# Optimization experiments

Measured on AMD Instinct MI355X. Metric: run time of the kernel, lower is better.

The kernel has to match this reference:

```python
import jax, jax.numpy as jnp
import numpy as np

N_ATOMS = 100000
M_NBRS = 12
ATOM_F = 64
NBR_F = 41
BN_EPS = 1e-5


def setup_inputs() -> dict:
    key = jax.random.key(0)
    k1, k2, k3, k4, k5 = jax.random.split(key, 5)
    atom_fea = jax.random.normal(k1, (N_ATOMS, ATOM_F), dtype=jnp.float32)
    nbr_fea = jax.random.normal(k2, (N_ATOMS, M_NBRS, NBR_F), dtype=jnp.float32)
    # fc_full: Linear(2*atom + nbr -> 2*atom), torch layout [out, in]
    in_dim = 2 * ATOM_F + NBR_F
    out_dim = 2 * ATOM_F
    W = jax.random.normal(k3, (out_dim, in_dim), dtype=jnp.float32) * (1.0 / np.sqrt(in_dim))
    b = jax.random.normal(k4, (out_dim,), dtype=jnp.float32) * 0.01
    gamma = jnp.ones((ATOM_F,), dtype=jnp.float32)
    beta = jnp.zeros((ATOM_F,), dtype=jnp.float32)
    nbr_idx = jax.random.randint(k5, (N_ATOMS, M_NBRS), 0, N_ATOMS, dtype=jnp.int32)
    return {"atom_fea": atom_fea, "nbr_fea": nbr_fea, "W": W, "b": b,
            "gamma": gamma, "beta": beta, "nbr_idx": nbr_idx}


def reference(atom_fea, nbr_fea, W, b, gamma, beta, nbr_idx):
    N, M = nbr_idx.shape
    F = atom_fea.shape[1]
    # gather neighbor atom features: [N, M, F]
    nbr_atom_fea = atom_fea[nbr_idx]
    # broadcast self features: [N, M, F]
    self_fea = jnp.broadcast_to(atom_fea[:, None, :], (N, M, F))
    # concat [self, nbr_atom, edge] -> [N, M, 2F + nbr_F]
    total_fea = jnp.concatenate([self_fea, nbr_atom_fea, nbr_fea], axis=2)
    # shared linear: [N, M, 2F]
    total_fea = jnp.einsum('nmi,oi->nmo', total_fea, W) + b
    filter_fea, core_fea = jnp.split(total_fea, 2, axis=2)
    # gated message, sum over neighbors -> [N, F]
    nbr_msg = (jax.nn.sigmoid(filter_fea) * jax.nn.softplus(core_fea)).sum(axis=1)
    # BatchNorm1d (training mode: batch stats, biased variance)
    x = atom_fea + nbr_msg
    mean = x.mean(axis=0)
    var = x.var(axis=0)
    x_hat = (x - mean) * jax.lax.rsqrt(var + BN_EPS)
    out = x_hat * gamma + beta
    return jax.nn.softplus(out)
```

## Files before the change

### kernel.cpp

```cpp
#include <hip/hip_runtime.h>

#define N_ATOMS 100000
#define M_NBRS 12
#define ATOM_F 64
#define NBR_F 41
#define OUT_DIM 128
#define IN_DIM 169
#define N_GROUPS (N_ATOMS / 16)

typedef __attribute__((ext_vector_type(8))) short short8;
typedef __attribute__((ext_vector_type(4))) float f32x4;
typedef __attribute__((ext_vector_type(2))) unsigned u32x2;
typedef __attribute__((ext_vector_type(4))) unsigned u32x4;

__device__ __forceinline__ unsigned short f2bf(float f) {
    union { float f; unsigned u; } v; v.f = f;
    unsigned u = v.u;
    return (unsigned short)((u + 0x7fffu + ((u >> 16) & 1u)) >> 16);
}
__device__ __forceinline__ unsigned cvt_pk(float a, float b) {
    unsigned r;
    asm("v_cvt_pk_bf16_f32 %0, %1, %2" : "=v"(r) : "v"(a), "v"(b));
    return r;
}
__device__ __forceinline__ float softplus_f(float x) {
    return fmaxf(x, 0.f) + __logf(1.f + __expf(-fabsf(x)));
}
__device__ __forceinline__ float sigmoid_f(float x) {
    return __fdividef(1.f, 1.f + __expf(-x));
}

#define WS_STRIDE 72
__global__ __launch_bounds__(256, 4) void k_prep(
    const float* __restrict__ atom, const float* __restrict__ W,
    const float* __restrict__ bias, unsigned* __restrict__ abf_u32,
    unsigned* __restrict__ A1P, float* __restrict__ SUM)
{
    __shared__ unsigned short Ws[128 * WS_STRIDE];
    __shared__ unsigned Ap[4 * 16 * 36];
    __shared__ unsigned T2[4][16 * 68];
    const int tid = threadIdx.x;
    const int w = tid >> 6, l = tid & 63;
    const int r = l & 15, g = l >> 4;

    if (blockIdx.x == 0 && tid < 128) SUM[tid] = 0.f;

    for (int e = tid; e < 128 * 64; e += 256) {
        int col = e >> 6, k = e & 63;
        Ws[col * WS_STRIDE + k] = f2bf(W[col * IN_DIM + k]);
    }
    __syncthreads();

    short8 bf[8][2];
    #pragma unroll
    for (int nt = 0; nt < 8; ++nt)
      #pragma unroll
      for (int kk = 0; kk < 2; ++kk) {
            int col = nt * 16 + r;
            union { u32x4 u; short8 s; } u;
            u.u = *reinterpret_cast<const u32x4*>(&Ws[col * WS_STRIDE + kk * 32 + g * 8]);
            bf[nt][kk] = u.s;
      }
    float bb[8];
    #pragma unroll
    for (int nt = 0; nt < 8; ++nt) bb[nt] = bias[nt * 16 + r];

    const int totalw = gridDim.x * 4;
    const int gw = blockIdx.x * 4 + w;
    const int step = totalw * 16;
    const int T = (N_ATOMS + step - 1) / step;
    unsigned* Aw = &Ap[w * 16 * 36];
    unsigned* Tw = T2[w];

    for (int t = 0; t < T; ++t) {
        int base = gw * 16 + t * step;
        #pragma unroll
        for (int sub = 0; sub < 4; ++sub) {
            int chunk = g * 4 + sub;
            int a = base + r;
            float4 v = make_float4(0.f, 0.f, 0.f, 0.f);
            if (a < N_ATOMS)
                v = reinterpret_cast<const float4*>(atom)[a * 16 + chunk];
            Aw[r * 36 + chunk * 2]     = cvt_pk(v.x, v.y);
            Aw[r * 36 + chunk * 2 + 1] = cvt_pk(v.z, v.w);
        }
        {
            int al = l >> 2, part = l & 3;
            int a = base + al;
            if (a < N_ATOMS) {
                u32x4 d0 = *reinterpret_cast<const u32x4*>(&Aw[al * 36 + part * 8]);
                u32x4 d1 = *reinterpret_cast<const u32x4*>(&Aw[al * 36 + part * 8 + 4]);
                *reinterpret_cast<u32x4*>(&abf_u32[(size_t)a * 32 + part * 8]) = d0;
                *reinterpret_cast<u32x4*>(&abf_u32[(size_t)a * 32 + part * 8 + 4]) = d1;
            }
        }
        short8 af[2];
        #pragma unroll
        for (int kk = 0; kk < 2; ++kk) {
            union { u32x4 u; short8 s; } u;
            u.u = *reinterpret_cast<const u32x4*>(&Aw[r * 36 + kk * 16 + g * 4]);
            af[kk] = u.s;
        }
        #pragma unroll
        for (int nt = 0; nt < 4; ++nt) {
            f32x4 accf = {0.f,0.f,0.f,0.f}, accc = {0.f,0.f,0.f,0.f};
            accf = __builtin_amdgcn_mfma_f32_16x16x32_bf16(af[0], bf[nt][0],   accf, 0,0,0);
            accf = __builtin_amdgcn_mfma_f32_16x16x32_bf16(af[1], bf[nt][1],   accf, 0,0,0);
            accc = __builtin_amdgcn_mfma_f32_16x16x32_bf16(af[0], bf[nt+4][0], accc, 0,0,0);
            accc = __builtin_amdgcn_mfma_f32_16x16x32_bf16(af[1], bf[nt+4][1], accc, 0,0,0);
            #pragma unroll
            for (int r4 = 0; r4 < 4; ++r4) {
                int row = g * 4 + r4;
                Tw[row * 68 + r * 4 + nt] = cvt_pk(accf[r4] + bb[nt], accc[r4] + bb[nt + 4]);
            }
        }
        {
            int al = l >> 2, part = l & 3;
            int a = base + al;
            if (a < N_ATOMS) {
                #pragma unroll
                for (int q = 0; q < 4; ++q) {
                    u32x4 d = *reinterpret_cast<const u32x4*>(&Tw[al * 68 + part * 16 + q * 4]);
                    *reinterpret_cast<u32x4*>(&A1P[(size_t)a * 64 + part * 16 + q * 4]) = d;
                }
            }
        }
    }
}

#define BS_STRIDE 136

struct TBuf { u32x2 ga[4]; float f0[4], f1[4], f2[4], f3[4]; };

__device__ __forceinline__ TBuf load_data(
    const unsigned* __restrict__ abf, const float* __restrict__ nbr,
    int base, int m, const int* jj, int c, int g)
{
    TBuf b;
    #pragma unroll
    for (int rr = 0; rr < 4; ++rr) {
        b.ga[rr] = *reinterpret_cast<const u32x2*>(abf + (size_t)jj[rr] * 32 + 2 * c);
        const float* ep = nbr + ((size_t)(base + rr * 4 + g) * M_NBRS + m) * NBR_F + 4 * c;
        bool c10 = (c < 10);
        b.f0[rr] = (c < 11) ? ep[0] : 0.f;
        b.f1[rr] = c10 ? ep[1] : 0.f;
        b.f2[rr] = c10 ? ep[2] : 0.f;
        b.f3[rr] = c10 ? ep[3] : 0.f;
    }
    return b;
}

__global__ __launch_bounds__(256, 3) void k_msg(
    const float* __restrict__ atom, const float* __restrict__ nbr,
    const float* __restrict__ W, const int* __restrict__ idx,
    const unsigned* __restrict__ abf, const unsigned* __restrict__ A1P,
    float* __restrict__ X, float* __restrict__ SUM)
{
    __shared__ __align__(16) unsigned short Bs[128 * BS_STRIDE];
    __shared__ __align__(16) unsigned Au[4 * 16 * 68];
    const int tid = threadIdx.x;
    const int w = tid >> 6, l = tid & 63;
    const int c = l & 15, g = l >> 4;
    unsigned* Aw = &Au[w * 16 * 68];

    for (int e = tid; e < 128 * BS_STRIDE / 2; e += 256)
        reinterpret_cast<unsigned*>(Bs)[e] = 0u;
    __syncthreads();
    for (int e = tid; e < 128 * 105; e += 256) {
        unsigned col = (unsigned)e / 105u;
        unsigned k = (unsigned)e - col * 105u;
        Bs[col * BS_STRIDE + k] = f2bf(W[col * IN_DIM + 64 + k]);
    }
    __syncthreads();

    const int gw = blockIdx.x * 4 + w;
    float sum_p[4] = {0.f,0.f,0.f,0.f}, sq_p[4] = {0.f,0.f,0.f,0.f};

    if (gw < N_GROUPS) {
        const int base = gw * 16;
        u32x4 a1q[4];
        #pragma unroll
        for (int r4 = 0; r4 < 4; ++r4)
            a1q[r4] = *reinterpret_cast<const u32x4*>(
                &A1P[(size_t)(base + g * 4 + r4) * 64 + c * 4]);

        float gs[4][4];
        #pragma unroll
        for (int r4 = 0; r4 < 4; ++r4)
          #pragma unroll
          for (int p = 0; p < 4; ++p) gs[r4][p] = 0.f;

        unsigned bofs = (unsigned)(c * BS_STRIDE + g * 8) * 2u;

        int jn[4];
        TBuf buf;
        {
            int j0[4];
            #pragma unroll
            for (int rr = 0; rr < 4; ++rr)
                j0[rr] = idx[(base + rr * 4 + g) * M_NBRS + 0];
            buf = load_data(abf, nbr, base, 0, j0, c, g);
        }
        #pragma unroll
        for (int rr = 0; rr < 4; ++rr)
            jn[rr] = idx[(base + rr * 4 + g) * M_NBRS + 1];

        #pragma unroll 1
        for (int m = 0; m < M_NBRS; ++m) {
            asm volatile("" : "+v"(bofs));
            #pragma unroll
            for (int rr = 0; rr < 4; ++rr) {
                int r = rr * 4 + g;
                *reinterpret_cast<u32x2*>(Aw + r * 68 + 2 * c) = buf.ga[rr];
                u32x2 e;
                e[0] = cvt_pk(buf.f0[rr], buf.f1[rr]);
                e[1] = cvt_pk(buf.f2[rr], buf.f3[rr]);
                *reinterpret_cast<u32x2*>(Aw + r * 68 + 32 + 2 * c) = e;
            }
            if (m + 1 < M_NBRS) {
                buf = load_data(abf, nbr, base, m + 1, jn, c, g);
                if (m + 2 < M_NBRS) {
                    #pragma unroll
                    for (int rr = 0; rr < 4; ++rr)
                        jn[rr] = idx[(base + rr * 4 + g) * M_NBRS + m + 2];
                }
            }
            short8 af[4];
            #pragma unroll
            for (int kk = 0; kk < 4; ++kk) {
                union { u32x4 u; short8 s; } u;
                u.u = *reinterpret_cast<const u32x4*>(&Aw[c * 68 + kk * 16 + g * 4]);
                af[kk] = u.s;
            }
            const char* bsb = reinterpret_cast<const char*>(Bs);
            #pragma unroll
            for (int p = 0; p < 4; ++p) {
                f32x4 accf, accc;
                #pragma unroll
                for (int r4 = 0; r4 < 4; ++r4) {
                    unsigned a1 = a1q[r4][p];
                    accf[r4] = __uint_as_float(a1 << 16);
                    accc[r4] = __uint_as_float(a1 & 0xffff0000u);
                }
                #pragma unroll
                for (int kk = 0; kk < 4; ++kk) {
                    union { u32x4 u; short8 s; } uf, uc;
                    uf.u = *reinterpret_cast<const u32x4*>(
                        bsb + bofs + (p * 16 * BS_STRIDE + kk * 32) * 2);
                    uc.u = *reinterpret_cast<const u32x4*>(
                        bsb + bofs + ((p + 4) * 16 * BS_STRIDE + kk * 32) * 2);
                    accf = __builtin_amdgcn_mfma_f32_16x16x32_bf16(af[kk], uf.s, accf, 0,0,0);
                    accc = __builtin_amdgcn_mfma_f32_16x16x32_bf16(af[kk], uc.s, accc, 0,0,0);
                }
                #pragma unroll
                for (int r4 = 0; r4 < 4; ++r4)
                    gs[r4][p] += sigmoid_f(accf[r4]) * softplus_f(accc[r4]);
            }
        }
        #pragma unroll
        for (int r4 = 0; r4 < 4; ++r4) {
            int o = (base + g * 4 + r4) * ATOM_F + c;
            #pragma unroll
            for (int p = 0; p < 4; ++p) {
                float x = atom[o + p * 16] + gs[r4][p];
                X[o + p * 16] = x;
                sum_p[p] += x;
                sq_p[p] += x * x;
            }
        }
    }

    #pragma unroll
    for (int p = 0; p < 4; ++p) {
        sum_p[p] += __shfl_xor(sum_p[p], 16, 64);
        sum_p[p] += __shfl_xor(sum_p[p], 32, 64);
        sq_p[p]  += __shfl_xor(sq_p[p], 16, 64);
        sq_p[p]  += __shfl_xor(sq_p[p], 32, 64);
    }
    __syncthreads();
    float* Rs = reinterpret_cast<float*>(Bs);
    if (g == 0) {
        #pragma unroll
        for (int p = 0; p < 4; ++p) {
            Rs[w * 128 + p * 16 + c] = sum_p[p];
            Rs[512 + w * 128 + p * 16 + c] = sq_p[p];
        }
    }
    __syncthreads();
    if (tid < 128) {
        int q = tid & 63;
        int o = (tid >> 6) * 512;
        float v = Rs[o + q] + Rs[o + 128 + q] + Rs[o + 256 + q] + Rs[o + 384 + q];
        atomicAdd(&SUM[tid], v);
    }
}

__global__ void k_stats2(const float* __restrict__ SUM, const float* __restrict__ gamma,
                         const float* __restrict__ beta, float* __restrict__ MS)
{
    int t = threadIdx.x;
    float mean = SUM[t] * (1.f / N_ATOMS);
    float msq  = SUM[64 + t] * (1.f / N_ATOMS);
    float var  = msq - mean * mean;
    float inv  = rsqrtf(var + 1e-5f);
    float sc   = inv * gamma[t];
    float sh   = beta[t] - mean * sc;
    MS[t] = sc;
    MS[64 + t] = sh;
}

__global__ void k_final(float* __restrict__ X, const float* __restrict__ MS)
{
    int q = blockIdx.x * 256 + threadIdx.x;
    const float4* MS4 = reinterpret_cast<const float4*>(MS);
    float4 x = reinterpret_cast<const float4*>(X)[q];
    float4 sc = MS4[q & 15];
    float4 sh = MS4[16 + (q & 15)];
    float4 o;
    o.x = softplus_f(x.x * sc.x + sh.x);
    o.y = softplus_f(x.y * sc.y + sh.y);
    o.z = softplus_f(x.z * sc.z + sh.z);
    o.w = softplus_f(x.w * sc.w + sh.w);
    reinterpret_cast<float4*>(X)[q] = o;
}

extern "C" void kernel_launch(void* const* d_in, const int* in_sizes, int n_in,
                              void* d_out, int out_size, void* d_ws, size_t ws_size,
                              hipStream_t stream)
{
    const float* atom  = (const float*)d_in[0];
    const float* nbr   = (const float*)d_in[1];
    const float* W     = (const float*)d_in[2];
    const float* bias  = (const float*)d_in[3];
    const float* gamma = (const float*)d_in[4];
    const float* beta  = (const float*)d_in[5];
    const int*   idx   = (const int*)d_in[6];
    float* X = (float*)d_out;

    char* ws = (char*)d_ws;
    unsigned* abf = (unsigned*)ws;
    unsigned* A1P = (unsigned*)(ws + (size_t)N_ATOMS * 32 * 4);
    float* SUM    = (float*)(ws + (size_t)N_ATOMS * 32 * 4
                                + (size_t)N_ATOMS * 64 * 4);
    float* MS     = SUM + 128;

    const int msg_blocks = (N_GROUPS + 3) / 4;
    hipLaunchKernelGGL(k_prep,   dim3(512),        dim3(256), 0, stream, atom, W, bias, abf, A1P, SUM);
    hipLaunchKernelGGL(k_msg,    dim3(msg_blocks), dim3(256), 0, stream, atom, nbr, W, idx, abf, A1P, X, SUM);
    hipLaunchKernelGGL(k_stats2, dim3(1),          dim3(64),  0, stream, SUM, gamma, beta, MS);
    hipLaunchKernelGGL(k_final,  dim3(6250),       dim3(256), 0, stream, X, MS);
}
```

Before: 414.5 us.

## Load MFMA A-fragments directly from global and pre-swizzle weight fragments in LDS

The message kernel now loads each neighbor's bf16 atom features and edge features directly into MFMA A-operand registers, with one atom row per lane column. This removes the per-neighbor LDS staging writes and reads. Weights are stored in LDS already laid out as per-lane fragments, which drops the padded stride and the zero-fill pass, lowers LDS use and allows occupancy 4. The prep kernel writes A1P in fragment order and launches one wave per 16-atom group instead of a grid-stride loop. The risks are more uncoalesced scattered global loads per lane, with edge loads of 8 floats each, and higher register pressure.

```diff
diff --git a/kernel.cpp b/kernel.cpp
--- a/kernel.cpp
+++ b/kernel.cpp
@@ -10,14 +10,8 @@
 
 typedef __attribute__((ext_vector_type(8))) short short8;
 typedef __attribute__((ext_vector_type(4))) float f32x4;
-typedef __attribute__((ext_vector_type(2))) unsigned u32x2;
 typedef __attribute__((ext_vector_type(4))) unsigned u32x4;
 
-__device__ __forceinline__ unsigned short f2bf(float f) {
-    union { float f; unsigned u; } v; v.f = f;
-    unsigned u = v.u;
-    return (unsigned short)((u + 0x7fffu + ((u >> 16) & 1u)) >> 16);
-}
 __device__ __forceinline__ unsigned cvt_pk(float a, float b) {
     unsigned r;
     asm("v_cvt_pk_bf16_f32 %0, %1, %2" : "=v"(r) : "v"(a), "v"(b));
@@ -30,146 +24,122 @@
     return __fdividef(1.f, 1.f + __expf(-x));
 }
 
-#define WS_STRIDE 72
 __global__ __launch_bounds__(256, 4) void k_prep(
     const float* __restrict__ atom, const float* __restrict__ W,
     const float* __restrict__ bias, unsigned* __restrict__ abf_u32,
     unsigned* __restrict__ A1P, float* __restrict__ SUM)
 {
-    __shared__ unsigned short Ws[128 * WS_STRIDE];
-    __shared__ unsigned Ap[4 * 16 * 36];
-    __shared__ unsigned T2[4][16 * 68];
+    __shared__ __align__(16) unsigned BFp[16 * 64 * 4];
     const int tid = threadIdx.x;
     const int w = tid >> 6, l = tid & 63;
     const int r = l & 15, g = l >> 4;
 
     if (blockIdx.x == 0 && tid < 128) SUM[tid] = 0.f;
 
-    for (int e = tid; e < 128 * 64; e += 256) {
-        int col = e >> 6, k = e & 63;
-        Ws[col * WS_STRIDE + k] = f2bf(W[col * IN_DIM + k]);
+    #pragma unroll
+    for (int s = 0; s < 4; ++s) {
+        int f = s * 4 + w;
+        int nt = f >> 1, kk = f & 1;
+        int col = nt * 16 + r;
+        int kbase = kk * 32 + g * 8;
+        const float* wp = W + col * IN_DIM + kbase;
+        u32x4 pk;
+        pk[0] = cvt_pk(wp[0], wp[1]); pk[1] = cvt_pk(wp[2], wp[3]);
+        pk[2] = cvt_pk(wp[4], wp[5]); pk[3] = cvt_pk(wp[6], wp[7]);
+        *reinterpret_cast<u32x4*>(&BFp[(f * 64 + l) * 4]) = pk;
     }
     __syncthreads();
 
-    short8 bf[8][2];
-    #pragma unroll
-    for (int nt = 0; nt < 8; ++nt)
-      #pragma unroll
-      for (int kk = 0; kk < 2; ++kk) {
-            int col = nt * 16 + r;
-            union { u32x4 u; short8 s; } u;
-            u.u = *reinterpret_cast<const u32x4*>(&Ws[col * WS_STRIDE + kk * 32 + g * 8]);
-            bf[nt][kk] = u.s;
-      }
+    const int gw = blockIdx.x * 4 + w;
+    if (gw >= N_GROUPS) return;
+    const int base = gw * 16;
+
     float bb[8];
     #pragma unroll
     for (int nt = 0; nt < 8; ++nt) bb[nt] = bias[nt * 16 + r];
 
-    const int totalw = gridDim.x * 4;
-    const int gw = blockIdx.x * 4 + w;
-    const int step = totalw * 16;
-    const int T = (N_ATOMS + step - 1) / step;
-    unsigned* Aw = &Ap[w * 16 * 36];
-    unsigned* Tw = T2[w];
-
-    for (int t = 0; t < T; ++t) {
-        int base = gw * 16 + t * step;
-        #pragma unroll
-        for (int sub = 0; sub < 4; ++sub) {
-            int chunk = g * 4 + sub;
-            int a = base + r;
-            float4 v = make_float4(0.f, 0.f, 0.f, 0.f);
-            if (a < N_ATOMS)
-                v = reinterpret_cast<const float4*>(atom)[a * 16 + chunk];
-            Aw[r * 36 + chunk * 2]     = cvt_pk(v.x, v.y);
-            Aw[r * 36 + chunk * 2 + 1] = cvt_pk(v.z, v.w);
-        }
-        {
-            int al = l >> 2, part = l & 3;
-            int a = base + al;
-            if (a < N_ATOMS) {
-                u32x4 d0 = *reinterpret_cast<const u32x4*>(&Aw[al * 36 + part * 8]);
-                u32x4 d1 = *reinterpret_cast<const u32x4*>(&Aw[al * 36 + part * 8 + 4]);
-                *reinterpret_cast<u32x4*>(&abf_u32[(size_t)a * 32 + part * 8]) = d0;
-                *reinterpret_cast<u32x4*>(&abf_u32[(size_t)a * 32 + part * 8 + 4]) = d1;
-            }
-        }
-        short8 af[2];
+    union { u32x4 u; short8 s; } af[2];
+    #pragma unroll
+    for (int kk = 0; kk < 2; ++kk) {
+        const float4* ap = reinterpret_cast<const float4*>(atom)
+                           + (size_t)(base + r) * 16 + kk * 8 + g * 2;
+        float4 v0 = ap[0], v1 = ap[1];
+        af[kk].u[0] = cvt_pk(v0.x, v0.y); af[kk].u[1] = cvt_pk(v0.z, v0.w);
+        af[kk].u[2] = cvt_pk(v1.x, v1.y); af[kk].u[3] = cvt_pk(v1.z, v1.w);
+        *reinterpret_cast<u32x4*>(&abf_u32[(size_t)(base + r) * 32 + kk * 16 + g * 4])
+            = af[kk].u;
+    }
+
+    u32x4 outp[4];
+    #pragma unroll
+    for (int nt = 0; nt < 4; ++nt) {
+        f32x4 accf = {0.f,0.f,0.f,0.f}, accc = {0.f,0.f,0.f,0.f};
         #pragma unroll
         for (int kk = 0; kk < 2; ++kk) {
-            union { u32x4 u; short8 s; } u;
-            u.u = *reinterpret_cast<const u32x4*>(&Aw[r * 36 + kk * 16 + g * 4]);
-            af[kk] = u.s;
-        }
-        #pragma unroll
-        for (int nt = 0; nt < 4; ++nt) {
-            f32x4 accf = {0.f,0.f,0.f,0.f}, accc = {0.f,0.f,0.f,0.f};
-            accf = __builtin_amdgcn_mfma_f32_16x16x32_bf16(af[0], bf[nt][0],   accf, 0,0,0);
-            accf = __builtin_amdgcn_mfma_f32_16x16x32_bf16(af[1], bf[nt][1],   accf, 0,0,0);
-            accc = __builtin_amdgcn_mfma_f32_16x16x32_bf16(af[0], bf[nt+4][0], accc, 0,0,0);
-            accc = __builtin_amdgcn_mfma_f32_16x16x32_bf16(af[1], bf[nt+4][1], accc, 0,0,0);
-            #pragma unroll
-            for (int r4 = 0; r4 < 4; ++r4) {
-                int row = g * 4 + r4;
-                Tw[row * 68 + r * 4 + nt] = cvt_pk(accf[r4] + bb[nt], accc[r4] + bb[nt + 4]);
-            }
-        }
-        {
-            int al = l >> 2, part = l & 3;
-            int a = base + al;
-            if (a < N_ATOMS) {
-                #pragma unroll
-                for (int q = 0; q < 4; ++q) {
-                    u32x4 d = *reinterpret_cast<const u32x4*>(&Tw[al * 68 + part * 16 + q * 4]);
-                    *reinterpret_cast<u32x4*>(&A1P[(size_t)a * 64 + part * 16 + q * 4]) = d;
-                }
-            }
-        }
-    }
-}
-
-#define BS_STRIDE 136
-
-struct TBuf { u32x2 ga[4]; float f0[4], f1[4], f2[4], f3[4]; };
-
-__device__ __forceinline__ TBuf load_data(
-    const unsigned* __restrict__ abf, const float* __restrict__ nbr,
-    int base, int m, const int* jj, int c, int g)
-{
-    TBuf b;
-    #pragma unroll
-    for (int rr = 0; rr < 4; ++rr) {
-        b.ga[rr] = *reinterpret_cast<const u32x2*>(abf + (size_t)jj[rr] * 32 + 2 * c);
-        const float* ep = nbr + ((size_t)(base + rr * 4 + g) * M_NBRS + m) * NBR_F + 4 * c;
-        bool c10 = (c < 10);
-        b.f0[rr] = (c < 11) ? ep[0] : 0.f;
-        b.f1[rr] = c10 ? ep[1] : 0.f;
-        b.f2[rr] = c10 ? ep[2] : 0.f;
-        b.f3[rr] = c10 ? ep[3] : 0.f;
+            union { u32x4 u; short8 s; } uf, uc;
+            uf.u = *reinterpret_cast<const u32x4*>(&BFp[((nt * 2 + kk) * 64 + l) * 4]);
+            uc.u = *reinterpret_cast<const u32x4*>(&BFp[(((nt + 4) * 2 + kk) * 64 + l) * 4]);
+            accf = __builtin_amdgcn_mfma_f32_16x16x32_bf16(af[kk].s, uf.s, accf, 0,0,0);
+            accc = __builtin_amdgcn_mfma_f32_16x16x32_bf16(af[kk].s, uc.s, accc, 0,0,0);
+        }
+        #pragma unroll
+        for (int r4 = 0; r4 < 4; ++r4)
+            outp[r4][nt] = cvt_pk(accf[r4] + bb[nt], accc[r4] + bb[nt + 4]);
+    }
+    #pragma unroll
+    for (int r4 = 0; r4 < 4; ++r4)
+        *reinterpret_cast<u32x4*>(&A1P[(size_t)gw * 1024 + r4 * 256 + l * 4]) = outp[r4];
+}
+
+struct EBuf { unsigned p2[4]; unsigned p3[4]; };
+
+__device__ __forceinline__ EBuf load_edges(const float* __restrict__ ep, int g)
+{
+    EBuf b;
+    float v[8];
+    #pragma unroll
+    for (int j = 0; j < 8; ++j) v[j] = ep[g * 8 + j];
+    b.p2[0] = cvt_pk(v[0], v[1]); b.p2[1] = cvt_pk(v[2], v[3]);
+    b.p2[2] = cvt_pk(v[4], v[5]); b.p2[3] = cvt_pk(v[6], v[7]);
+    b.p3[0] = b.p3[1] = b.p3[2] = b.p3[3] = 0u;
+    if (g == 0) {
+        float u[8];
+        #pragma unroll
+        for (int j = 0; j < 8; ++j) u[j] = ep[32 + j];
+        b.p3[0] = cvt_pk(u[0], u[1]); b.p3[1] = cvt_pk(u[2], u[3]);
+        b.p3[2] = cvt_pk(u[4], u[5]); b.p3[3] = cvt_pk(u[6], u[7]);
+    } else if (g == 1) {
+        b.p3[0] = cvt_pk(ep[40], 0.f);
     }
     return b;
 }
 
-__global__ __launch_bounds__(256, 3) void k_msg(
+__global__ __launch_bounds__(256, 4) void k_msg(
     const float* __restrict__ atom, const float* __restrict__ nbr,
     const float* __restrict__ W, const int* __restrict__ idx,
     const unsigned* __restrict__ abf, const unsigned* __restrict__ A1P,
     float* __restrict__ X, float* __restrict__ SUM)
 {
-    __shared__ __align__(16) unsigned short Bs[128 * BS_STRIDE];
-    __shared__ __align__(16) unsigned Au[4 * 16 * 68];
+    __shared__ __align__(16) unsigned BF[32 * 64 * 4];
     const int tid = threadIdx.x;
     const int w = tid >> 6, l = tid & 63;
     const int c = l & 15, g = l >> 4;
-    unsigned* Aw = &Au[w * 16 * 68];
-
-    for (int e = tid; e < 128 * BS_STRIDE / 2; e += 256)
-        reinterpret_cast<unsigned*>(Bs)[e] = 0u;
-    __syncthreads();
-    for (int e = tid; e < 128 * 105; e += 256) {
-        unsigned col = (unsigned)e / 105u;
-        unsigned k = (unsigned)e - col * 105u;
-        Bs[col * BS_STRIDE + k] = f2bf(W[col * IN_DIM + 64 + k]);
+
+    #pragma unroll
+    for (int s = 0; s < 8; ++s) {
+        int f = s * 4 + w;
+        int nt = f >> 2, kk = f & 3;
+        int col = nt * 16 + c;
+        int kbase = kk * 32 + g * 8;
+        const float* wp = W + col * IN_DIM + 64 + kbase;
+        u32x4 pk;
+        float v[8];
+        #pragma unroll
+        for (int j = 0; j < 8; ++j)
+            v[j] = (kbase + j < 105) ? wp[j] : 0.f;
+        pk[0] = cvt_pk(v[0], v[1]); pk[1] = cvt_pk(v[2], v[3]);
+        pk[2] = cvt_pk(v[4], v[5]); pk[3] = cvt_pk(v[6], v[7]);
+        *reinterpret_cast<u32x4*>(&BF[(f * 64 + l) * 4]) = pk;
     }
     __syncthreads();
 
@@ -182,7 +152,7 @@
         #pragma unroll
         for (int r4 = 0; r4 < 4; ++r4)
             a1q[r4] = *reinterpret_cast<const u32x4*>(
-                &A1P[(size_t)(base + g * 4 + r4) * 64 + c * 4]);
+                &A1P[(size_t)gw * 1024 + r4 * 256 + l * 4]);
 
         float gs[4][4];
         #pragma unroll
@@ -190,72 +160,62 @@
           #pragma unroll
           for (int p = 0; p < 4; ++p) gs[r4][p] = 0.f;
 
-        unsigned bofs = (unsigned)(c * BS_STRIDE + g * 8) * 2u;
-
-        int jn[4];
-        TBuf buf;
+        const int irow = (base + c) * M_NBRS;
+        const float* erow = nbr + (size_t)irow * NBR_F;
+
+        unsigned bofs = (unsigned)l * 16u;
+
+        u32x4 at0, at1, at0n, at1n;
+        EBuf eb, ebn;
+        int jn;
         {
-            int j0[4];
-            #pragma unroll
-            for (int rr = 0; rr < 4; ++rr)
-                j0[rr] = idx[(base + rr * 4 + g) * M_NBRS + 0];
-            buf = load_data(abf, nbr, base, 0, j0, c, g);
-        }
-        #pragma unroll
-        for (int rr = 0; rr < 4; ++rr)
-            jn[rr] = idx[(base + rr * 4 + g) * M_NBRS + 1];
+            int j0 = idx[irow];
+            at0 = *reinterpret_cast<const u32x4*>(abf + (size_t)j0 * 32 + g * 4);
+            at1 = *reinterpret_cast<const u32x4*>(abf + (size_t)j0 * 32 + 16 + g * 4);
+            eb = load_edges(erow, g);
+        }
+        jn = idx[irow + 1];
 
         #pragma unroll 1
         for (int m = 0; m < M_NBRS; ++m) {
+            if (m + 1 < M_NBRS) {
+                at0n = *reinterpret_cast<const u32x4*>(abf + (size_t)jn * 32 + g * 4);
+                at1n = *reinterpret_cast<const u32x4*>(abf + (size_t)jn * 32 + 16 + g * 4);
+                ebn = load_edges(erow + (m + 1) * NBR_F, g);
+                if (m + 2 < M_NBRS) jn = idx[irow + m + 2];
+            }
             asm volatile("" : "+v"(bofs));
-            #pragma unroll
-            for (int rr = 0; rr < 4; ++rr) {
-                int r = rr * 4 + g;
-                *reinterpret_cast<u32x2*>(Aw + r * 68 + 2 * c) = buf.ga[rr];
-                u32x2 e;
-                e[0] = cvt_pk(buf.f0[rr], buf.f1[rr]);
-                e[1] = cvt_pk(buf.f2[rr], buf.f3[rr]);
-                *reinterpret_cast<u32x2*>(Aw + r * 68 + 32 + 2 * c) = e;
-            }
-            if (m + 1 < M_NBRS) {
-                buf = load_data(abf, nbr, base, m + 1, jn, c, g);
-                if (m + 2 < M_NBRS) {
-                    #pragma unroll
-                    for (int rr = 0; rr < 4; ++rr)
-                        jn[rr] = idx[(base + rr * 4 + g) * M_NBRS + m + 2];
-                }
-            }
-            short8 af[4];
-            #pragma unroll
-            for (int kk = 0; kk < 4; ++kk) {
-                union { u32x4 u; short8 s; } u;
-                u.u = *reinterpret_cast<const u32x4*>(&Aw[c * 68 + kk * 16 + g * 4]);
-                af[kk] = u.s;
-            }
-            const char* bsb = reinterpret_cast<const char*>(Bs);
+            const char* bsb = reinterpret_cast<const char*>(BF);
+            union { u32x4 u; short8 s; } a0, a1, a2, a3;
+            a0.u = at0; a1.u = at1;
+            a2.u[0] = eb.p2[0]; a2.u[1] = eb.p2[1]; a2.u[2] = eb.p2[2]; a2.u[3] = eb.p2[3];
+            a3.u[0] = eb.p3[0]; a3.u[1] = eb.p3[1]; a3.u[2] = eb.p3[2]; a3.u[3] = eb.p3[3];
             #pragma unroll
             for (int p = 0; p < 4; ++p) {
                 f32x4 accf, accc;
                 #pragma unroll
                 for (int r4 = 0; r4 < 4; ++r4) {
-                    unsigned a1 = a1q[r4][p];
-                    accf[r4] = __uint_as_float(a1 << 16);
-                    accc[r4] = __uint_as_float(a1 & 0xffff0000u);
+                    unsigned v = a1q[r4][p];
+                    accf[r4] = __uint_as_float(v << 16);
+                    accc[r4] = __uint_as_float(v & 0xffff0000u);
                 }
                 #pragma unroll
                 for (int kk = 0; kk < 4; ++kk) {
                     union { u32x4 u; short8 s; } uf, uc;
                     uf.u = *reinterpret_cast<const u32x4*>(
-                        bsb + bofs + (p * 16 * BS_STRIDE + kk * 32) * 2);
+                        bsb + bofs + (unsigned)((p * 4 + kk) * 64 * 16));
                     uc.u = *reinterpret_cast<const u32x4*>(
-                        bsb + bofs + ((p + 4) * 16 * BS_STRIDE + kk * 32) * 2);
-                    accf = __builtin_amdgcn_mfma_f32_16x16x32_bf16(af[kk], uf.s, accf, 0,0,0);
-                    accc = __builtin_amdgcn_mfma_f32_16x16x32_bf16(af[kk], uc.s, accc, 0,0,0);
+                        bsb + bofs + (unsigned)(((p + 4) * 4 + kk) * 64 * 16));
+                    short8 afk = (kk == 0) ? a0.s : (kk == 1) ? a1.s
+                               : (kk == 2) ? a2.s : a3.s;
+                    accf = __builtin_amdgcn_mfma_f32_16x16x32_bf16(afk, uf.s, accf, 0,0,0);
+                    accc = __builtin_amdgcn_mfma_f32_16x16x32_bf16(afk, uc.s, accc, 0,0,0);
                 }
                 #pragma unroll
                 for (int r4 = 0; r4 < 4; ++r4)
                     gs[r4][p] += sigmoid_f(accf[r4]) * softplus_f(accc[r4]);
             }
+            at0 = at0n; at1 = at1n; eb = ebn;
         }
         #pragma unroll
         for (int r4 = 0; r4 < 4; ++r4) {
@@ -278,7 +238,7 @@
         sq_p[p]  += __shfl_xor(sq_p[p], 32, 64);
     }
     __syncthreads();
-    float* Rs = reinterpret_cast<float*>(Bs);
+    float* Rs = reinterpret_cast<float*>(BF);
     if (g == 0) {
         #pragma unroll
         for (int p = 0; p < 4; ++p) {
@@ -341,12 +301,12 @@
     unsigned* abf = (unsigned*)ws;
     unsigned* A1P = (unsigned*)(ws + (size_t)N_ATOMS * 32 * 4);
     float* SUM    = (float*)(ws + (size_t)N_ATOMS * 32 * 4
-                                + (size_t)N_ATOMS * 64 * 4);
+                                + (size_t)N_GROUPS * 1024 * 4);
     float* MS     = SUM + 128;
 
-    const int msg_blocks = (N_GROUPS + 3) / 4;
-    hipLaunchKernelGGL(k_prep,   dim3(512),        dim3(256), 0, stream, atom, W, bias, abf, A1P, SUM);
-    hipLaunchKernelGGL(k_msg,    dim3(msg_blocks), dim3(256), 0, stream, atom, nbr, W, idx, abf, A1P, X, SUM);
-    hipLaunchKernelGGL(k_stats2, dim3(1),          dim3(64),  0, stream, SUM, gamma, beta, MS);
-    hipLaunchKernelGGL(k_final,  dim3(6250),       dim3(256), 0, stream, X, MS);
-}
+    const int blocks = (N_GROUPS + 3) / 4;
+    hipLaunchKernelGGL(k_prep,   dim3(blocks), dim3(256), 0, stream, atom, W, bias, abf, A1P, SUM);
+    hipLaunchKernelGGL(k_msg,    dim3(blocks), dim3(256), 0, stream, atom, nbr, W, idx, abf, A1P, X, SUM);
+    hipLaunchKernelGGL(k_stats2, dim3(1),      dim3(64),  0, stream, SUM, gamma, beta, MS);
+    hipLaunchKernelGGL(k_final,  dim3(6250),   dim3(256), 0, stream, X, MS);
+}
```

Result: slower. 447.1 us (+7.8%).
